# Optimization experiments

Measured on AMD Instinct MI355X. Metric: run time of the kernel, lower is better.

Reference implementation:

```python
import jax, jax.numpy as jnp
import numpy as np

N = 100000      # nodes
F = 128         # feature dim == LSTM hidden dim (num_inputs)
E = 1600000     # edges (avg degree 16)
KARY = 8        # max neighbors per node fed to the LSTM
NPERMS = 4      # eval-time permutations (self.training == False)
NOUT = 64       # num_outputs


def setup_inputs() -> dict:
    key = jax.random.key(0)
    ks = jax.random.split(key, 8)
    s = 0.05
    node_feat = jax.random.normal(ks[0], (N, F), dtype=jnp.float32)
    adjacency = jax.random.randint(ks[1], (E, 2), 0, N, dtype=jnp.int32)
    # LSTM params, torch gate order (i, f, g, o)
    w_ih = jax.random.normal(ks[2], (4 * F, F), dtype=jnp.float32) * s
    w_hh = jax.random.normal(ks[3], (4 * F, F), dtype=jnp.float32) * s
    b_ih = jax.random.normal(ks[4], (4 * F,), dtype=jnp.float32) * s
    b_hh = jax.random.normal(ks[5], (4 * F,), dtype=jnp.float32) * s
    weight = jax.random.normal(ks[6], (2 * F, NOUT), dtype=jnp.float32) * s
    bias = jax.random.normal(ks[7], (NOUT,), dtype=jnp.float32) * s
    return {"node_feat": node_feat, "adjacency": adjacency, "w_ih": w_ih,
            "w_hh": w_hh, "b_ih": b_ih, "b_hh": b_hh,
            "weight": weight, "bias": bias}


def _padded_neighbors(adjacency, perm_key):
    """Random-sample up to KARY neighbors per node (random order), vectorized.
    Returns padded neighbor indices [N, KARY] (-1 pad) and lengths [N]."""
    src, dst = adjacency[:, 0], adjacency[:, 1]
    e = src.shape[0]
    deg = jax.ops.segment_sum(jnp.ones((e,), jnp.int32), src, num_segments=N)
    offsets = jnp.cumsum(deg) - deg  # start of each node's edge block
    r = jax.random.uniform(perm_key, (e,))
    order = jnp.lexsort((r, src))    # sort by src, random tiebreak -> random perm per node
    s2, d2 = src[order], dst[order]
    rank = jnp.arange(e, dtype=jnp.int32) - offsets[s2]  # position within node's list
    slot = jnp.where(rank < KARY, rank, KARY)            # overflow -> dump column
    padded = jnp.full((N, KARY + 1), -1, jnp.int32)
    padded = padded.at[s2, slot].set(d2)
    return padded[:, :KARY], jnp.minimum(deg, KARY)


def _lstm_cn(feats, lengths, w_ih, w_hh, b_ih, b_hh):
    """Masked LSTM over padded sequences; returns final cell state c_n [N, F]
    (state frozen once t >= length, matching pack_padded_sequence semantics)."""
    n, k, f = feats.shape

    def step(carry, inp):
        h, c = carry
        x, t = inp  # x: [n, f]
        gates = x @ w_ih.T + b_ih + h @ w_hh.T + b_hh  # [n, 4f]
        i, fg, g, o = jnp.split(gates, 4, axis=-1)
        i, fg, o = jax.nn.sigmoid(i), jax.nn.sigmoid(fg), jax.nn.sigmoid(o)
        g = jnp.tanh(g)
        c_new = fg * c + i * g
        h_new = o * jnp.tanh(c_new)
        m = (t < lengths)[:, None]
        return (jnp.where(m, h_new, h), jnp.where(m, c_new, c)), None

    init = (jnp.zeros((n, f), feats.dtype), jnp.zeros((n, f), feats.dtype))
    xs = (jnp.swapaxes(feats, 0, 1), jnp.arange(k, dtype=jnp.int32))
    (_, c), _ = jax.lax.scan(step, init, xs)
    return c


def reference(node_feat, adjacency, w_ih, w_hh, b_ih, b_hh, weight, bias):
    key = jax.random.key(42)
    h_neigh = jnp.zeros_like(node_feat)
    for p in range(NPERMS):  # small fixed count, not a data dim
        idx, lengths = _padded_neighbors(adjacency, jax.random.fold_in(key, p))
        feats = node_feat[jnp.maximum(idx, 0)]  # [N, KARY, F]; padding masked via lengths
        h_neigh = h_neigh + _lstm_cn(feats, lengths, w_ih, w_hh, b_ih, b_hh)
    h_neigh = h_neigh * (1.0 / NPERMS)
    return jax.nn.sigmoid(jnp.concatenate([node_feat, h_neigh], axis=1) @ weight + bias)
```

## Files before the change

### kernel.cpp

```cpp
#include <hip/hip_runtime.h>
#include <stdint.h>

#define N_NODES 100000
#define F 128
#define E_EDGES 1600000
#define KARY 8
#define NPERMS 4
#define NOUT 64

typedef __attribute__((ext_vector_type(8))) short bf16x8;
typedef __attribute__((ext_vector_type(4))) float f32x4;

__device__ __forceinline__ uint32_t rotl32(uint32_t v, int r) {
  return (v << r) | (v >> (32 - r));
}
__device__ __forceinline__ void tf2x32(uint32_t k0, uint32_t k1, uint32_t& x0, uint32_t& x1) {
  uint32_t ks2 = k0 ^ k1 ^ 0x1BD11BDAu;
  x0 += k0; x1 += k1;
  x0 += x1; x1 = rotl32(x1,13); x1 ^= x0;
  x0 += x1; x1 = rotl32(x1,15); x1 ^= x0;
  x0 += x1; x1 = rotl32(x1,26); x1 ^= x0;
  x0 += x1; x1 = rotl32(x1, 6); x1 ^= x0;
  x0 += k1; x1 += ks2 + 1u;
  x0 += x1; x1 = rotl32(x1,17); x1 ^= x0;
  x0 += x1; x1 = rotl32(x1,29); x1 ^= x0;
  x0 += x1; x1 = rotl32(x1,16); x1 ^= x0;
  x0 += x1; x1 = rotl32(x1,24); x1 ^= x0;
  x0 += ks2; x1 += k0 + 2u;
  x0 += x1; x1 = rotl32(x1,13); x1 ^= x0;
  x0 += x1; x1 = rotl32(x1,15); x1 ^= x0;
  x0 += x1; x1 = rotl32(x1,26); x1 ^= x0;
  x0 += x1; x1 = rotl32(x1, 6); x1 ^= x0;
  x0 += k0; x1 += k1 + 3u;
  x0 += x1; x1 = rotl32(x1,17); x1 ^= x0;
  x0 += x1; x1 = rotl32(x1,29); x1 ^= x0;
  x0 += x1; x1 = rotl32(x1,16); x1 ^= x0;
  x0 += x1; x1 = rotl32(x1,24); x1 ^= x0;
  x0 += k1; x1 += ks2 + 4u;
  x0 += x1; x1 = rotl32(x1,13); x1 ^= x0;
  x0 += x1; x1 = rotl32(x1,15); x1 ^= x0;
  x0 += x1; x1 = rotl32(x1,26); x1 ^= x0;
  x0 += x1; x1 = rotl32(x1, 6); x1 ^= x0;
  x0 += ks2; x1 += k0 + 5u;
}

__device__ __forceinline__ unsigned short f2bf(float f) {
  uint32_t u = __float_as_uint(f);
  uint32_t r = (u + 0x7FFFu + ((u >> 16) & 1u)) >> 16;
  return (unsigned short)r;
}
__device__ __forceinline__ float ubf(uint32_t u) { return __uint_as_float(u); }
__device__ __forceinline__ uint32_t cvtpk(float lo, float hi) {
  uint32_t r;
  asm("v_cvt_pk_bf16_f32 %0, %1, %2" : "=v"(r) : "v"(lo), "v"(hi));
  return r;
}

__device__ __forceinline__ f32x4 exp2v(f32x4 x) {
  f32x4 r;
  r.x = __builtin_amdgcn_exp2f(x.x);
  r.y = __builtin_amdgcn_exp2f(x.y);
  r.z = __builtin_amdgcn_exp2f(x.z);
  r.w = __builtin_amdgcn_exp2f(x.w);
  return r;
}
__device__ __forceinline__ f32x4 rcpv(f32x4 x) {
  f32x4 r;
  r.x = __builtin_amdgcn_rcpf(x.x);
  r.y = __builtin_amdgcn_rcpf(x.y);
  r.z = __builtin_amdgcn_rcpf(x.z);
  r.w = __builtin_amdgcn_rcpf(x.w);
  return r;
}
__device__ __forceinline__ f32x4 sig4p(f32x4 y) {
  return rcpv(1.0f + exp2v(y));
}
__device__ __forceinline__ f32x4 tanh4p2(f32x4 y) {
  return 1.0f - 2.0f * rcpv(exp2v(y) + 1.0f);
}
__device__ __forceinline__ f32x4 tanh4(f32x4 x) {
  return 1.0f - 2.0f * rcpv(exp2v(x * 2.88539008f) + 1.0f);
}
__device__ __forceinline__ float sigf(float x) {
  return __builtin_amdgcn_rcpf(1.0f + __builtin_amdgcn_exp2f(x * -1.44269504f));
}

#define GSC -1.44269504f
#define GSC_G 2.88539008f

#define HIST_BLK (E_EDGES / 256)

__global__ __launch_bounds__(256) void k_hist_prepw(
    const int2* __restrict__ adj, int* __restrict__ deg,
    const float* __restrict__ w_ih, const float* __restrict__ w_hh,
    const float* __restrict__ b_ih, const float* __restrict__ b_hh,
    const float* __restrict__ weight,
    short* __restrict__ wihb, short* __restrict__ whb,
    float4* __restrict__ bq, short* __restrict__ wobT) {
  int b = blockIdx.x;
  if (b < HIST_BLK) {
    int e = b * 256 + threadIdx.x;
    atomicAdd(&deg[adj[e].x], 1);
  } else {
    int t = (b - HIST_BLK) * 256 + threadIdx.x;
    float sc = ((t >> 14) == 2) ? GSC_G : GSC;
    wihb[t] = (short)f2bf(w_ih[t] * sc);
    whb[t] = (short)f2bf(w_hh[t] * sc);
    if (t < 2 * F * NOUT) {
      int n = t & 63, k = t >> 6;
      wobT[n * 256 + k] = (short)f2bf(weight[k * NOUT + n]);
    }
    if (t < F)
      bq[t] = make_float4(GSC * (b_ih[t] + b_hh[t]), GSC * (b_ih[F + t] + b_hh[F + t]),
                          GSC_G * (b_ih[2 * F + t] + b_hh[2 * F + t]),
                          GSC * (b_ih[3 * F + t] + b_hh[3 * F + t]));
  }
}

__global__ __launch_bounds__(1024) void k_scanA(const int* __restrict__ deg,
                                                int* __restrict__ rpart,
                                                int* __restrict__ bsum) {
  __shared__ int s[1024];
  int tid = threadIdx.x;
  int i = blockIdx.x * 1024 + tid;
  int v = (i < N_NODES) ? deg[i] : 0;
  s[tid] = v;
  __syncthreads();
  for (int off = 1; off < 1024; off <<= 1) {
    int t = (tid >= off) ? s[tid - off] : 0;
    __syncthreads();
    s[tid] += t;
    __syncthreads();
  }
  if (i < N_NODES) rpart[i] = s[tid] - v;
  if (tid == 1023) bsum[blockIdx.x] = s[tid];
}

__global__ __launch_bounds__(128) void k_scanB(const int* __restrict__ bsum,
                                               int* __restrict__ boff) {
  __shared__ int s[128];
  int tid = threadIdx.x;
  int v = (tid < 98) ? bsum[tid] : 0;
  s[tid] = v;
  __syncthreads();
  for (int off = 1; off < 128; off <<= 1) {
    int t = (tid >= off) ? s[tid - off] : 0;
    __syncthreads();
    s[tid] += t;
    __syncthreads();
  }
  if (tid < 98) boff[tid] = s[tid] - v;
}

__global__ void k_scatter(const int2* __restrict__ adj, const int* __restrict__ rpart,
                          const int* __restrict__ boff, int* __restrict__ cursor,
                          int2* __restrict__ csr) {
  int e = blockIdx.x * blockDim.x + threadIdx.x;
  if (e < E_EDGES) {
    int2 a = adj[e];
    int pos = rpart[a.x] + boff[a.x >> 10] + atomicAdd(&cursor[a.x], 1);
    csr[pos] = make_int2(a.y, e);
  }
}

#define HS_LD 136
#define SEL_BLK ((N_NODES + 255) / 256)

__global__ __launch_bounds__(256) void k_sel_xg(
    const int2* __restrict__ csr, const int* __restrict__ rpart,
    const int* __restrict__ boff,
    const int* __restrict__ deg, int* __restrict__ sel, int* __restrict__ lens,
    const float* __restrict__ feat, const short* __restrict__ wihb,
    const float4* __restrict__ bq, ushort4* __restrict__ xgq) {
  __shared__ short as_[32 * HS_LD];
  if (blockIdx.x < SEL_BLK) {
    int n = blockIdx.x * 256 + threadIdx.x;
    if (n >= N_NODES) return;
    uint32_t pk0[NPERMS], pk1[NPERMS];
#pragma unroll
    for (int p = 0; p < NPERMS; ++p) {
      uint32_t a = 0u, b = (uint32_t)p;
      tf2x32(0u, 42u, a, b);
      pk0[p] = a; pk1[p] = b;
    }
    int off = rpart[n] + boff[n >> 10], d = deg[n];
    unsigned long long key[NPERMS][KARY];
    int nbr[NPERMS][KARY];
#pragma unroll
    for (int p = 0; p < NPERMS; ++p)
#pragma unroll
      for (int i = 0; i < KARY; ++i) { key[p][i] = ~0ULL; nbr[p][i] = -1; }
    for (int e = 0; e < d; ++e) {
      int2 ent = csr[off + e];
#pragma unroll
      for (int p = 0; p < NPERMS; ++p) {
        uint32_t x0 = 0u, x1 = (uint32_t)ent.y;
        tf2x32(pk0[p], pk1[p], x0, x1);
        uint32_t bits = x0 ^ x1;
        unsigned long long k = ((unsigned long long)(bits >> 9) << 21) | (unsigned)ent.y;
        if (k < key[p][KARY - 1]) {
          key[p][KARY - 1] = k; nbr[p][KARY - 1] = ent.x;
#pragma unroll
          for (int s = KARY - 1; s >= 1; --s) {
            if (key[p][s] < key[p][s - 1]) {
              unsigned long long tk = key[p][s]; key[p][s] = key[p][s - 1]; key[p][s - 1] = tk;
              int tn = nbr[p][s]; nbr[p][s] = nbr[p][s - 1]; nbr[p][s - 1] = tn;
            }
          }
        }
      }
    }
    int L = d < KARY ? d : KARY;
    lens[n] = L;
#pragma unroll
    for (int p = 0; p < NPERMS; ++p)
#pragma unroll
      for (int t = 0; t < KARY; ++t)
        sel[((size_t)p * N_NODES + n) * KARY + t] = (t < L) ? nbr[p][t] : -1;
  } else {
    const int tid = threadIdx.x;
    const int w = tid >> 6, l = tid & 63;
    const int l15 = l & 15, q = l >> 4;
    const int nb = (blockIdx.x - SEL_BLK) * 32;
#pragma unroll
    for (int i = 0; i < 4; ++i) {
      int idx = tid + i * 256;
      int row = idx >> 5, c4 = (idx & 31) * 4;
      float4 v = *(const float4*)&feat[(size_t)(nb + row) * F + c4];
      ushort4 s;
      s.x = f2bf(v.x); s.y = f2bf(v.y); s.z = f2bf(v.z); s.w = f2bf(v.w);
      *(ushort4*)&as_[row * HS_LD + c4] = s;
    }
    __syncthreads();

    f32x4 acc[2][2][4];
#pragma unroll
    for (int mt = 0; mt < 2; ++mt)
#pragma unroll
      for (int ft = 0; ft < 2; ++ft)
#pragma unroll
        for (int g4 = 0; g4 < 4; ++g4) acc[mt][ft][g4] = (f32x4){0.f, 0.f, 0.f, 0.f};

    const short* ab = as_ + l15 * HS_LD + q * 8;
#pragma unroll
    for (int kt = 0; kt < 4; ++kt) {
      bf16x8 a0 = *(const bf16x8*)(ab + kt * 32);
      bf16x8 a1 = *(const bf16x8*)(ab + 16 * HS_LD + kt * 32);
#pragma unroll
      for (int g4 = 0; g4 < 4; ++g4)
#pragma unroll
        for (int ft = 0; ft < 2; ++ft) {
          bf16x8 b = *(const bf16x8*)(wihb + (size_t)(g4 * 128 + 16 * ft + 32 * w + l15) * F + q * 8 + kt * 32);
          acc[0][ft][g4] = __builtin_amdgcn_mfma_f32_16x16x32_bf16(a0, b, acc[0][ft][g4], 0, 0, 0);
          acc[1][ft][g4] = __builtin_amdgcn_mfma_f32_16x16x32_bf16(a1, b, acc[1][ft][g4], 0, 0, 0);
        }
    }
#pragma unroll
    for (int mt = 0; mt < 2; ++mt)
#pragma unroll
      for (int ft = 0; ft < 2; ++ft) {
        int fi = 32 * w + 16 * ft + l15;
        float4 bb = bq[fi];
#pragma unroll
        for (int r = 0; r < 4; ++r) {
          int node = nb + mt * 16 + q * 4 + r;
          ushort4 o;
          o.x = f2bf(acc[mt][ft][0][r] + bb.x);
          o.y = f2bf(acc[mt][ft][1][r] + bb.y);
          o.z = f2bf(acc[mt][ft][2][r] + bb.z);
          o.w = f2bf(acc[mt][ft][3][r] + bb.w);
          xgq[(size_t)node * F + (l15 + 16 * w) * 2 + ft] = o;
        }
      }
  }
}

#define LB 8
#define OS_LD 264
__global__ __launch_bounds__(256, 2) void k_lstm(const short* __restrict__ whb,
                                                 const ushort4* __restrict__ xgq,
                                                 const int* __restrict__ sel,
                                                 const int* __restrict__ lens,
                                                 const float* __restrict__ feat,
                                                 const short* __restrict__ wobT,
                                                 const float* __restrict__ bias,
                                                 float* __restrict__ out) {
  __shared__ short hs[2][32 * HS_LD];
  __shared__ int sel_l[32][9];
  const int tid = threadIdx.x;
  const int w = tid >> 6;
  const int l = tid & 63;
  const int l15 = l & 15, q = l >> 4;
  const int nb = blockIdx.x * LB;
  const char* xgb = (const char*)xgq;
  const int fi16 = (16 * w + l15) * 16;

  {
    int m = tid >> 3, t = tid & 7;
    int node = nb + (m >> 2), p = m & 3;
    sel_l[m][t] = sel[((size_t)p * N_NODES + node) * KARY + t];
  }
  {
    int* h32 = (int*)hs;
    for (int i = tid; i < 32 * HS_LD; i += 256) h32[i] = 0;
  }
  uint32_t lp = 0;
#pragma unroll
  for (int i = 0; i < 8; ++i) lp |= (uint32_t)lens[nb + i] << (4 * i);

  bf16x8 breg[4][4][2];
#pragma unroll
  for (int kt = 0; kt < 4; ++kt)
#pragma unroll
    for (int g4 = 0; g4 < 4; ++g4)
#pragma unroll
      for (int ft = 0; ft < 2; ++ft)
        breg[kt][g4][ft] = *(const bf16x8*)(whb + (size_t)(g4 * 128 + 16 * ft + 32 * w + l15) * F + q * 8 + kt * 32);

  const short* ab0 = hs[0] + l15 * HS_LD + q * 8;
  const short* ab1 = hs[1] + l15 * HS_LD + q * 8;

  f32x4 cst[2][2];
#pragma unroll
  for (int mt = 0; mt < 2; ++mt)
#pragma unroll
    for (int ft = 0; ft < 2; ++ft) cst[mt][ft] = (f32x4){0.f, 0.f, 0.f, 0.f};

  __syncthreads();

  auto lstm_step = [&](int t, const short* abase, short* hw) {
    uint4 xr[2][4];
#pragma unroll
    for (int mt = 0; mt < 2; ++mt)
#pragma unroll
      for (int r = 0; r < 4; ++r) {
        int seq = mt * 16 + q * 4 + r;
        int v = sel_l[seq][t];
        v = v < 0 ? 0 : v;
        xr[mt][r] = *(const uint4*)(xgb + (v << 10) + fi16);
      }

    f32x4 acc[2][2][4];
#pragma unroll
    for (int mt = 0; mt < 2; ++mt)
#pragma unroll
      for (int r = 0; r < 4; ++r) {
        uint4 x = xr[mt][r];
        acc[mt][0][0][r] = ubf(x.x << 16);
        acc[mt][0][1][r] = ubf(x.x & 0xffff0000u);
        acc[mt][0][2][r] = ubf(x.y << 16);
        acc[mt][0][3][r] = ubf(x.y & 0xffff0000u);
        acc[mt][1][0][r] = ubf(x.z << 16);
        acc[mt][1][1][r] = ubf(x.z & 0xffff0000u);
        acc[mt][1][2][r] = ubf(x.w << 16);
        acc[mt][1][3][r] = ubf(x.w & 0xffff0000u);
      }

#pragma unroll
    for (int kt = 0; kt < 4; ++kt) {
      bf16x8 a0 = *(const bf16x8*)(abase + 0 * 16 * HS_LD + kt * 32);
      bf16x8 a1 = *(const bf16x8*)(abase + 1 * 16 * HS_LD + kt * 32);
#pragma unroll
      for (int g4 = 0; g4 < 4; ++g4)
#pragma unroll
        for (int ft = 0; ft < 2; ++ft) {
          acc[0][ft][g4] = __builtin_amdgcn_mfma_f32_16x16x32_bf16(a0, breg[kt][g4][ft], acc[0][ft][g4], 0, 0, 0);
          acc[1][ft][g4] = __builtin_amdgcn_mfma_f32_16x16x32_bf16(a1, breg[kt][g4][ft], acc[1][ft][g4], 0, 0, 0);
        }
    }

#pragma unroll
    for (int mt = 0; mt < 2; ++mt) {
      int len = (lp >> (4 * (mt * 4 + q))) & 15;
      bool live = t < len;
#pragma unroll
      for (int ft = 0; ft < 2; ++ft) {
        f32x4 ii = sig4p(acc[mt][ft][0]);
        f32x4 ff = sig4p(acc[mt][ft][1]);
        f32x4 gg = tanh4p2(acc[mt][ft][2]);
        f32x4 oo = sig4p(acc[mt][ft][3]);
        f32x4 cn = ff * cst[mt][ft] + ii * gg;
        if (live) {
          cst[mt][ft] = cn;
          f32x4 hh = oo * tanh4(cn);
          int base = (mt * 16 + q * 4) * HS_LD + 32 * w + 16 * ft + l15;
          uint32_t p01 = cvtpk(hh[0], hh[1]);
          uint32_t p23 = cvtpk(hh[2], hh[3]);
          hw[base + 0 * HS_LD] = (short)p01;
          hw[base + 1 * HS_LD] = (short)(p01 >> 16);
          hw[base + 2 * HS_LD] = (short)p23;
          hw[base + 3 * HS_LD] = (short)(p23 >> 16);
        }
      }
    }
    __syncthreads();
  };

  for (int tt = 0; tt < KARY; tt += 2) {
    lstm_step(tt, ab0, hs[1]);
    lstm_step(tt + 1, ab1, hs[0]);
  }

  short* as2 = hs[0];

#pragma unroll
  for (int mt = 0; mt < 2; ++mt)
#pragma unroll
    for (int ft = 0; ft < 2; ++ft) {
      f32x4 cc = cst[mt][ft];
      float hv = (cc.x + cc.y + cc.z + cc.w) * 0.25f;
      as2[(mt * 4 + q) * OS_LD + 128 + 32 * w + 16 * ft + l15] = (short)f2bf(hv);
    }
  {
    int row = tid >> 5, c4 = (tid & 31) * 4;
    float4 v = *(const float4*)&feat[(size_t)(nb + row) * F + c4];
    ushort4 s;
    s.x = f2bf(v.x); s.y = f2bf(v.y); s.z = f2bf(v.z); s.w = f2bf(v.w);
    *(ushort4*)&as2[row * OS_LD + c4] = s;
  }
  float bb = bias[16 * w + l15];
  __syncthreads();

  f32x4 oacc = (f32x4){0.f, 0.f, 0.f, 0.f};
  const short* ab2 = as2 + l15 * OS_LD + q * 8;
#pragma unroll
  for (int kt = 0; kt < 8; ++kt) {
    bf16x8 a = *(const bf16x8*)(ab2 + kt * 32);
    bf16x8 b = *(const bf16x8*)(wobT + (size_t)(16 * w + l15) * 256 + q * 8 + kt * 32);
    oacc = __builtin_amdgcn_mfma_f32_16x16x32_bf16(a, b, oacc, 0, 0, 0);
  }
  if (q < 2) {
#pragma unroll
    for (int r = 0; r < 4; ++r) {
      int node = nb + q * 4 + r;
      out[(size_t)node * NOUT + 16 * w + l15] = sigf(oacc[r] + bb);
    }
  }
}

extern "C" void kernel_launch(void* const* d_in, const int* in_sizes, int n_in,
                              void* d_out, int out_size, void* d_ws, size_t ws_size,
                              hipStream_t stream) {
  const float* feat = (const float*)d_in[0];
  const int2* adj = (const int2*)d_in[1];
  const float* w_ih = (const float*)d_in[2];
  const float* w_hh = (const float*)d_in[3];
  const float* b_ih = (const float*)d_in[4];
  const float* b_hh = (const float*)d_in[5];
  const float* weight = (const float*)d_in[6];
  const float* bias = (const float*)d_in[7];
  float* out = (float*)d_out;

  size_t off = 0;
  auto take = [&](size_t bytes) -> void* {
    void* p = (char*)d_ws + off;
    off += (bytes + 255) & ~(size_t)255;
    return p;
  };
  int* deg = (int*)take((size_t)N_NODES * 4);
  int* rpart = (int*)take((size_t)N_NODES * 4);
  int* cursor = (int*)take((size_t)N_NODES * 4);
  int2* csr = (int2*)take((size_t)E_EDGES * 8);
  int* sel = (int*)take((size_t)NPERMS * N_NODES * KARY * 4);
  int* lens = (int*)take((size_t)N_NODES * 4);
  short* wihb = (short*)take((size_t)4 * F * F * 2);
  short* whb = (short*)take((size_t)4 * F * F * 2);
  short* wobT = (short*)take((size_t)NOUT * 2 * F * 2);
  float4* bq = (float4*)take((size_t)F * 16);
  ushort4* xgq = (ushort4*)take((size_t)N_NODES * F * 8);
  int* bsum = (int*)take(128 * 4);
  int* boff = (int*)take(128 * 4);
  (void)ws_size; (void)in_sizes; (void)n_in; (void)out_size;

  hipMemsetAsync(deg, 0, (size_t)N_NODES * 4, stream);
  hipMemsetAsync(cursor, 0, (size_t)N_NODES * 4, stream);

  k_hist_prepw<<<HIST_BLK + 256, 256, 0, stream>>>(adj, deg, w_ih, w_hh, b_ih, b_hh,
                                                   weight, wihb, whb, bq, wobT);
  k_scanA<<<98, 1024, 0, stream>>>(deg, rpart, bsum);
  k_scanB<<<1, 128, 0, stream>>>(bsum, boff);
  k_scatter<<<(E_EDGES + 255) / 256, 256, 0, stream>>>(adj, rpart, boff, cursor, csr);
  k_sel_xg<<<SEL_BLK + N_NODES / 32, 256, 0, stream>>>(csr, rpart, boff, deg, sel, lens,
                                                       feat, wihb, bq, xgq);
  k_lstm<<<N_NODES / LB, 256, 0, stream>>>(whb, xgq, sel, lens, feat, wobT, bias, out);
}
```

Before: 1.211 ms.

## Split LSTM recurrence across 8 waves with one feature tile each

Doubles the LSTM block to 512 threads so each wave owns one 16-feature tile instead of two. This halves per-thread recurrent weight registers and accumulators, and launch bounds are raised to allow more resident waves. The xg layout is changed so each wave reads 8-byte rows, and the output gate and h write are skipped on the final timestep since only c_n is used. Half the waves sit idle during the output projection, and the larger block means more threads take part in each per-step barrier.

```diff
diff --git a/kernel.cpp b/kernel.cpp
--- a/kernel.cpp
+++ b/kernel.cpp
@@ -269,7 +269,7 @@
           o.y = f2bf(acc[mt][ft][1][r] + bb.y);
           o.z = f2bf(acc[mt][ft][2][r] + bb.z);
           o.w = f2bf(acc[mt][ft][3][r] + bb.w);
-          xgq[(size_t)node * F + (l15 + 16 * w) * 2 + ft] = o;
+          xgq[(size_t)node * F + fi] = o;
         }
       }
   }
@@ -277,7 +277,7 @@
 
 #define LB 8
 #define OS_LD 264
-__global__ __launch_bounds__(256, 2) void k_lstm(const short* __restrict__ whb,
+__global__ __launch_bounds__(512, 4) void k_lstm(const short* __restrict__ whb,
                                                  const ushort4* __restrict__ xgq,
                                                  const int* __restrict__ sel,
                                                  const int* __restrict__ lens,
@@ -293,43 +293,39 @@
   const int l15 = l & 15, q = l >> 4;
   const int nb = blockIdx.x * LB;
   const char* xgb = (const char*)xgq;
-  const int fi16 = (16 * w + l15) * 16;
-
-  {
+  const int fi8 = (16 * w + l15) * 8;
+
+  if (tid < 256) {
     int m = tid >> 3, t = tid & 7;
     int node = nb + (m >> 2), p = m & 3;
     sel_l[m][t] = sel[((size_t)p * N_NODES + node) * KARY + t];
   }
   {
     int* h32 = (int*)hs;
-    for (int i = tid; i < 32 * HS_LD; i += 256) h32[i] = 0;
+    for (int i = tid; i < 32 * HS_LD; i += 512) h32[i] = 0;
   }
   uint32_t lp = 0;
 #pragma unroll
   for (int i = 0; i < 8; ++i) lp |= (uint32_t)lens[nb + i] << (4 * i);
 
-  bf16x8 breg[4][4][2];
+  bf16x8 breg[4][4];
 #pragma unroll
   for (int kt = 0; kt < 4; ++kt)
 #pragma unroll
     for (int g4 = 0; g4 < 4; ++g4)
-#pragma unroll
-      for (int ft = 0; ft < 2; ++ft)
-        breg[kt][g4][ft] = *(const bf16x8*)(whb + (size_t)(g4 * 128 + 16 * ft + 32 * w + l15) * F + q * 8 + kt * 32);
+      breg[kt][g4] = *(const bf16x8*)(whb + (size_t)(g4 * 128 + 16 * w + l15) * F + q * 8 + kt * 32);
 
   const short* ab0 = hs[0] + l15 * HS_LD + q * 8;
   const short* ab1 = hs[1] + l15 * HS_LD + q * 8;
 
-  f32x4 cst[2][2];
-#pragma unroll
-  for (int mt = 0; mt < 2; ++mt)
-#pragma unroll
-    for (int ft = 0; ft < 2; ++ft) cst[mt][ft] = (f32x4){0.f, 0.f, 0.f, 0.f};
+  f32x4 cst[2];
+  cst[0] = (f32x4){0.f, 0.f, 0.f, 0.f};
+  cst[1] = (f32x4){0.f, 0.f, 0.f, 0.f};
 
   __syncthreads();
 
   auto lstm_step = [&](int t, const short* abase, short* hw) {
-    uint4 xr[2][4];
+    uint2 xr[2][4];
 #pragma unroll
     for (int mt = 0; mt < 2; ++mt)
 #pragma unroll
@@ -337,23 +333,19 @@
         int seq = mt * 16 + q * 4 + r;
         int v = sel_l[seq][t];
         v = v < 0 ? 0 : v;
-        xr[mt][r] = *(const uint4*)(xgb + (v << 10) + fi16);
-      }
-
-    f32x4 acc[2][2][4];
+        xr[mt][r] = *(const uint2*)(xgb + (v << 10) + fi8);
+      }
+
+    f32x4 acc[2][4];
 #pragma unroll
     for (int mt = 0; mt < 2; ++mt)
 #pragma unroll
       for (int r = 0; r < 4; ++r) {
-        uint4 x = xr[mt][r];
-        acc[mt][0][0][r] = ubf(x.x << 16);
-        acc[mt][0][1][r] = ubf(x.x & 0xffff0000u);
-        acc[mt][0][2][r] = ubf(x.y << 16);
-        acc[mt][0][3][r] = ubf(x.y & 0xffff0000u);
-        acc[mt][1][0][r] = ubf(x.z << 16);
-        acc[mt][1][1][r] = ubf(x.z & 0xffff0000u);
-        acc[mt][1][2][r] = ubf(x.w << 16);
-        acc[mt][1][3][r] = ubf(x.w & 0xffff0000u);
+        uint2 x = xr[mt][r];
+        acc[mt][0][r] = ubf(x.x << 16);
+        acc[mt][1][r] = ubf(x.x & 0xffff0000u);
+        acc[mt][2][r] = ubf(x.y << 16);
+        acc[mt][3][r] = ubf(x.y & 0xffff0000u);
       }
 
 #pragma unroll
@@ -361,29 +353,26 @@
       bf16x8 a0 = *(const bf16x8*)(abase + 0 * 16 * HS_LD + kt * 32);
       bf16x8 a1 = *(const bf16x8*)(abase + 1 * 16 * HS_LD + kt * 32);
 #pragma unroll
-      for (int g4 = 0; g4 < 4; ++g4)
-#pragma unroll
-        for (int ft = 0; ft < 2; ++ft) {
-          acc[0][ft][g4] = __builtin_amdgcn_mfma_f32_16x16x32_bf16(a0, breg[kt][g4][ft], acc[0][ft][g4], 0, 0, 0);
-          acc[1][ft][g4] = __builtin_amdgcn_mfma_f32_16x16x32_bf16(a1, breg[kt][g4][ft], acc[1][ft][g4], 0, 0, 0);
-        }
+      for (int g4 = 0; g4 < 4; ++g4) {
+        acc[0][g4] = __builtin_amdgcn_mfma_f32_16x16x32_bf16(a0, breg[kt][g4], acc[0][g4], 0, 0, 0);
+        acc[1][g4] = __builtin_amdgcn_mfma_f32_16x16x32_bf16(a1, breg[kt][g4], acc[1][g4], 0, 0, 0);
+      }
     }
 
 #pragma unroll
     for (int mt = 0; mt < 2; ++mt) {
       int len = (lp >> (4 * (mt * 4 + q))) & 15;
       bool live = t < len;
-#pragma unroll
-      for (int ft = 0; ft < 2; ++ft) {
-        f32x4 ii = sig4p(acc[mt][ft][0]);
-        f32x4 ff = sig4p(acc[mt][ft][1]);
-        f32x4 gg = tanh4p2(acc[mt][ft][2]);
-        f32x4 oo = sig4p(acc[mt][ft][3]);
-        f32x4 cn = ff * cst[mt][ft] + ii * gg;
-        if (live) {
-          cst[mt][ft] = cn;
+      f32x4 ii = sig4p(acc[mt][0]);
+      f32x4 ff = sig4p(acc[mt][1]);
+      f32x4 gg = tanh4p2(acc[mt][2]);
+      f32x4 cn = ff * cst[mt] + ii * gg;
+      if (live) {
+        cst[mt] = cn;
+        if (t < KARY - 1) {
+          f32x4 oo = sig4p(acc[mt][3]);
           f32x4 hh = oo * tanh4(cn);
-          int base = (mt * 16 + q * 4) * HS_LD + 32 * w + 16 * ft + l15;
+          int base = (mt * 16 + q * 4) * HS_LD + 16 * w + l15;
           uint32_t p01 = cvtpk(hh[0], hh[1]);
           uint32_t p23 = cvtpk(hh[2], hh[3]);
           hw[base + 0 * HS_LD] = (short)p01;
@@ -404,36 +393,36 @@
   short* as2 = hs[0];
 
 #pragma unroll
-  for (int mt = 0; mt < 2; ++mt)
-#pragma unroll
-    for (int ft = 0; ft < 2; ++ft) {
-      f32x4 cc = cst[mt][ft];
-      float hv = (cc.x + cc.y + cc.z + cc.w) * 0.25f;
-      as2[(mt * 4 + q) * OS_LD + 128 + 32 * w + 16 * ft + l15] = (short)f2bf(hv);
-    }
-  {
+  for (int mt = 0; mt < 2; ++mt) {
+    f32x4 cc = cst[mt];
+    float hv = (cc.x + cc.y + cc.z + cc.w) * 0.25f;
+    as2[(mt * 4 + q) * OS_LD + 128 + 16 * w + l15] = (short)f2bf(hv);
+  }
+  if (tid < 256) {
     int row = tid >> 5, c4 = (tid & 31) * 4;
     float4 v = *(const float4*)&feat[(size_t)(nb + row) * F + c4];
     ushort4 s;
     s.x = f2bf(v.x); s.y = f2bf(v.y); s.z = f2bf(v.z); s.w = f2bf(v.w);
     *(ushort4*)&as2[row * OS_LD + c4] = s;
   }
-  float bb = bias[16 * w + l15];
+  float bb = (w < 4) ? bias[16 * w + l15] : 0.f;
   __syncthreads();
 
-  f32x4 oacc = (f32x4){0.f, 0.f, 0.f, 0.f};
-  const short* ab2 = as2 + l15 * OS_LD + q * 8;
-#pragma unroll
-  for (int kt = 0; kt < 8; ++kt) {
-    bf16x8 a = *(const bf16x8*)(ab2 + kt * 32);
-    bf16x8 b = *(const bf16x8*)(wobT + (size_t)(16 * w + l15) * 256 + q * 8 + kt * 32);
-    oacc = __builtin_amdgcn_mfma_f32_16x16x32_bf16(a, b, oacc, 0, 0, 0);
-  }
-  if (q < 2) {
-#pragma unroll
-    for (int r = 0; r < 4; ++r) {
-      int node = nb + q * 4 + r;
-      out[(size_t)node * NOUT + 16 * w + l15] = sigf(oacc[r] + bb);
+  if (w < 4) {
+    f32x4 oacc = (f32x4){0.f, 0.f, 0.f, 0.f};
+    const short* ab2 = as2 + l15 * OS_LD + q * 8;
+#pragma unroll
+    for (int kt = 0; kt < 8; ++kt) {
+      bf16x8 a = *(const bf16x8*)(ab2 + kt * 32);
+      bf16x8 b = *(const bf16x8*)(wobT + (size_t)(16 * w + l15) * 256 + q * 8 + kt * 32);
+      oacc = __builtin_amdgcn_mfma_f32_16x16x32_bf16(a, b, oacc, 0, 0, 0);
+    }
+    if (q < 2) {
+#pragma unroll
+      for (int r = 0; r < 4; ++r) {
+        int node = nb + q * 4 + r;
+        out[(size_t)node * NOUT + 16 * w + l15] = sigf(oacc[r] + bb);
+      }
     }
   }
 }
@@ -482,5 +471,5 @@
   k_scatter<<<(E_EDGES + 255) / 256, 256, 0, stream>>>(adj, rpart, boff, cursor, csr);
   k_sel_xg<<<SEL_BLK + N_NODES / 32, 256, 0, stream>>>(csr, rpart, boff, deg, sel, lens,
                                                        feat, wihb, bq, xgq);
-  k_lstm<<<N_NODES / LB, 256, 0, stream>>>(whb, xgq, sel, lens, feat, wobT, bias, out);
-}
+  k_lstm<<<N_NODES / LB, 512, 0, stream>>>(whb, xgq, sel, lens, feat, wobT, bias, out);
+}
```

Result: slower. 1.492 ms (+23.2%).
